# Kernel optimization log

Measured on AMD Instinct MI355X. Metric: run time of the kernel, lower is better.

Reference implementation:

```python
import jax, jax.numpy as jnp
import numpy as np

N = 50000      # nodes
E = 800000     # edges
IN = 128       # in_channels
HID = 64       # hidden_channels (out per head)
H = 4          # heads
ED = 64        # edge_dim
HC = H * HID   # concat output width


def segment_softmax(logits, seg, num_segments):
    # logits: [E, H], softmax over edges sharing the same destination node
    m = jax.ops.segment_max(logits, seg, num_segments=num_segments)
    m = jnp.where(jnp.isfinite(m), m, 0.0)
    e = jnp.exp(logits - m[seg])
    s = jax.ops.segment_sum(e, seg, num_segments=num_segments)
    return e / (s[seg] + 1e-16)


def gatv2_layer(x, src, dst, edge_attr, Wl, bl, Wr, br, We, att, bias):
    # GATv2Conv (PyG, concat=True, negative_slope=0.2), dropout off (eval)
    Hh, C = att.shape
    xl = (x @ Wl + bl).reshape(-1, Hh, C)   # [N,H,C] source transform
    xr = (x @ Wr + br).reshape(-1, Hh, C)   # [N,H,C] target transform
    ee = (edge_attr @ We).reshape(-1, Hh, C)  # [E,H,C]
    m = jax.nn.leaky_relu(xl[src] + xr[dst] + ee, 0.2)  # [E,H,C]
    logits = jnp.einsum('ehc,hc->eh', m, att)           # [E,H]
    alpha = segment_softmax(logits, dst, x.shape[0])    # [E,H]
    out = jax.ops.segment_sum(alpha[:, :, None] * xl[src], dst,
                              num_segments=x.shape[0])  # [N,H,C]
    return out.reshape(x.shape[0], Hh * C) + bias


def setup_inputs() -> dict:
    key = jax.random.key(0)
    ks = jax.random.split(key, 20)
    g = lambda k, shape, s=0.05: (jax.random.normal(k, shape, jnp.float32) * s)
    inp = {
        'x': jax.random.normal(ks[0], (N, IN), jnp.float32),
        'edge_index': jax.random.randint(ks[1], (2, E), 0, N, dtype=jnp.int32),
        'edge_attr': jax.random.normal(ks[2], (E, ED), jnp.float32),
        # layer 1: in_channels -> heads*hidden
        'Wl1': g(ks[3], (IN, HC)), 'bl1': jnp.zeros((HC,), jnp.float32),
        'Wr1': g(ks[4], (IN, HC)), 'br1': jnp.zeros((HC,), jnp.float32),
        'We1': g(ks[5], (ED, HC)),
        'att1': g(ks[6], (H, HID)), 'bias1': jnp.zeros((HC,), jnp.float32),
        # layer 2: heads*hidden -> heads*hidden
        'Wl2': g(ks[7], (HC, HC)), 'bl2': jnp.zeros((HC,), jnp.float32),
        'Wr2': g(ks[8], (HC, HC)), 'br2': jnp.zeros((HC,), jnp.float32),
        'We2': g(ks[9], (ED, HC)),
        'att2': g(ks[10], (H, HID)), 'bias2': jnp.zeros((HC,), jnp.float32),
    }
    return inp


def reference(x, edge_index, edge_attr,
              Wl1, bl1, Wr1, br1, We1, att1, bias1,
              Wl2, bl2, Wr2, br2, We2, att2, bias2):
    src, dst = edge_index[0], edge_index[1]
    h1 = gatv2_layer(x, src, dst, edge_attr, Wl1, bl1, Wr1, br1, We1, att1, bias1)
    h2 = gatv2_layer(h1, src, dst, edge_attr, Wl2, bl2, Wr2, br2, We2, att2, bias2)
    return h2
```

## Files before the change

### kernel.cpp

```cpp
#include <hip/hip_runtime.h>
#include <math.h>

#define NN 50000
#define NE 800000

#define LRELU(v) fmaxf((v), 0.2f * (v))

typedef __attribute__((ext_vector_type(4))) float f32x4;
typedef __attribute__((ext_vector_type(8))) short bf16x8;

static __device__ __forceinline__ unsigned short f2bf(float f) {
  union { float f; unsigned int i; } c; c.f = f;
  unsigned int r = c.i + 0x7fff + ((c.i >> 16) & 1);
  return (unsigned short)(r >> 16);
}
static __device__ __forceinline__ float bflo(unsigned int u) {
  union { unsigned int i; float f; } c; c.i = u << 16; return c.f;
}
static __device__ __forceinline__ float bfhi(unsigned int u) {
  union { unsigned int i; float f; } c; c.i = u & 0xffff0000u; return c.f;
}

__global__ __launch_bounds__(256)
void conv_all(const float* __restrict__ We1, unsigned short* __restrict__ wef1,
              const float* __restrict__ We2, unsigned short* __restrict__ wef2,
              const float* __restrict__ Wl1, unsigned short* __restrict__ wlf1,
              const float* __restrict__ Wr1, unsigned short* __restrict__ wrf1,
              const float* __restrict__ Wl2, unsigned short* __restrict__ wlf2,
              const float* __restrict__ Wr2, unsigned short* __restrict__ wrf2) {
  const int y = blockIdx.y;
  const int g = blockIdx.x * 256 + threadIdx.x;
  if (y < 2) {
    if (g >= 16384) return;
    const float* We = y ? We2 : We1;
    unsigned short* wef = y ? wef2 : wef1;
    const int j = g & 7;
    const int l = (g >> 3) & 63;
    const int t = g >> 9;
    const int n = t & 15, half = t >> 4;
    const int k = half * 32 + (l >> 4) * 8 + j;
    const int c = ((l & 15) >> 2) * 64 + n * 4 + (l & 3);
    wef[g] = f2bf(We[(size_t)k * 256 + c]);
  } else {
    const int K = (y < 4) ? 128 : 256;
    if (g >= K * 256) return;
    const float* W = (y == 2) ? Wl1 : (y == 3) ? Wr1 : (y == 4) ? Wl2 : Wr2;
    unsigned short* wf = (y == 2) ? wlf1 : (y == 3) ? wrf1
                       : (y == 4) ? wlf2 : wrf2;
    const int j = g & 7;
    const int l = (g >> 3) & 63;
    const int fn = g >> 9;
    const int n = fn & 15, ks = fn >> 4;
    const int k = ks * 32 + (l >> 4) * 8 + j;
    const int c = n * 16 + (l & 15);
    wf[g] = f2bf(W[(size_t)k * 256 + c]);
  }
}

template <int KS>
__global__ __launch_bounds__(256)
void gemm_mfma2(const float* __restrict__ A,
                const unsigned short* __restrict__ wfl,
                const float* __restrict__ bl, unsigned short* __restrict__ outl,
                const unsigned short* __restrict__ wfr,
                const float* __restrict__ br, unsigned short* __restrict__ outr) {
  const int tid = threadIdx.x;
  const int w = tid >> 6, l = tid & 63;
  const int lid = l & 15, lg = l >> 4;
  const int row  = blockIdx.x * 64 + w * 16 + lid;
  const bool rowok = row < NN;
  const int rowv = rowok ? row : NN - 1;
  const int K = KS * 32;

  bf16x8 bfr[KS];
  const float* ap = A + (size_t)rowv * K + lg * 8;
#pragma unroll
  for (int ks = 0; ks < KS; ++ks) {
    const float4 v0 = *(const float4*)(ap + ks * 32);
    const float4 v1 = *(const float4*)(ap + ks * 32 + 4);
    bf16x8 b;
    b[0]=f2bf(v0.x); b[1]=f2bf(v0.y); b[2]=f2bf(v0.z); b[3]=f2bf(v0.w);
    b[4]=f2bf(v1.x); b[5]=f2bf(v1.y); b[6]=f2bf(v1.z); b[7]=f2bf(v1.w);
    bfr[ks] = b;
  }

  f32x4 acc[16];

#pragma unroll
  for (int n = 0; n < 16; ++n) acc[n] = (f32x4){0.f, 0.f, 0.f, 0.f};
#pragma unroll
  for (int ks = 0; ks < KS; ++ks)
#pragma unroll
    for (int n = 0; n < 16; ++n) {
      const bf16x8 a = *(const bf16x8*)(wfl + ((size_t)(ks * 16 + n) * 64 + l) * 8);
      acc[n] = __builtin_amdgcn_mfma_f32_16x16x32_bf16(a, bfr[ks], acc[n], 0, 0, 0);
    }
  if (rowok) {
#pragma unroll
    for (int n = 0; n < 16; ++n) {
      const int c0 = n * 16 + lg * 4;
      const float4 bv = *(const float4*)(bl + c0);
      ushort4 o;
      o.x = f2bf(acc[n][0] + bv.x); o.y = f2bf(acc[n][1] + bv.y);
      o.z = f2bf(acc[n][2] + bv.z); o.w = f2bf(acc[n][3] + bv.w);
      *(ushort4*)(outl + (size_t)row * 256 + c0) = o;
    }
  }

#pragma unroll
  for (int n = 0; n < 16; ++n) acc[n] = (f32x4){0.f, 0.f, 0.f, 0.f};
#pragma unroll
  for (int ks = 0; ks < KS; ++ks)
#pragma unroll
    for (int n = 0; n < 16; ++n) {
      const bf16x8 a = *(const bf16x8*)(wfr + ((size_t)(ks * 16 + n) * 64 + l) * 8);
      acc[n] = __builtin_amdgcn_mfma_f32_16x16x32_bf16(a, bfr[ks], acc[n], 0, 0, 0);
    }
  if (rowok) {
#pragma unroll
    for (int n = 0; n < 16; ++n) {
      const int c0 = n * 16 + lg * 4;
      const float4 bv = *(const float4*)(br + c0);
      ushort4 o;
      o.x = f2bf(acc[n][0] + bv.x); o.y = f2bf(acc[n][1] + bv.y);
      o.z = f2bf(acc[n][2] + bv.z); o.w = f2bf(acc[n][3] + bv.w);
      *(ushort4*)(outr + (size_t)row * 256 + c0) = o;
    }
  }
}

__global__ __launch_bounds__(256)
void dst_hist(const int* __restrict__ dst, int* __restrict__ cnt) {
  const int e = blockIdx.x * 256 + threadIdx.x;
  if (e < NE) atomicAdd(&cnt[dst[e]], 1);
}

__global__ __launch_bounds__(1024)
void scan_bsum(const int* __restrict__ cnt, int* __restrict__ bsum, int n) {
  __shared__ int wsum[16];
  const int tid = threadIdx.x;
  const int lane = tid & 63, wid = tid >> 6;
  const int i = blockIdx.x * 1024 + tid;
  int v = (i < n) ? cnt[i] : 0;
#pragma unroll
  for (int off = 32; off >= 1; off >>= 1) v += __shfl_xor(v, off);
  if (lane == 0) wsum[wid] = v;
  __syncthreads();
  if (tid == 0) {
    int s = 0;
#pragma unroll
    for (int k = 0; k < 16; ++k) s += wsum[k];
    bsum[blockIdx.x] = s;
  }
}

__global__ __launch_bounds__(64)
void scan_bsum_scan(int* __restrict__ bsum, int* __restrict__ row_start,
                    int nb, int n) {
  const int lane = threadIdx.x;
  const int v = (lane < nb) ? bsum[lane] : 0;
  int incl = v;
#pragma unroll
  for (int off = 1; off < 64; off <<= 1) {
    const int t = __shfl_up(incl, off);
    if (lane >= off) incl += t;
  }
  if (lane < nb) bsum[lane] = incl - v;
  if (lane == 63) row_start[n] = incl;
}

__global__ __launch_bounds__(1024)
void scan_apply(int* __restrict__ cnt, const int* __restrict__ bsum,
                int* __restrict__ row_start, int n) {
  __shared__ int wsum[16];
  __shared__ int woff[16];
  const int tid = threadIdx.x;
  const int lane = tid & 63, wid = tid >> 6;
  const int i = blockIdx.x * 1024 + tid;
  const int v = (i < n) ? cnt[i] : 0;
  int incl = v;
#pragma unroll
  for (int off = 1; off < 64; off <<= 1) {
    const int t = __shfl_up(incl, off);
    if (lane >= off) incl += t;
  }
  if (lane == 63) wsum[wid] = incl;
  __syncthreads();
  if (wid == 0) {
    const int s = (lane < 16) ? wsum[lane] : 0;
    int si = s;
#pragma unroll
    for (int off = 1; off < 16; off <<= 1) {
      const int t = __shfl_up(si, off);
      if (lane >= off) si += t;
    }
    if (lane < 16) woff[lane] = si - s;
  }
  __syncthreads();
  if (i < n) {
    const int excl = bsum[blockIdx.x] + woff[wid] + incl - v;
    row_start[i] = excl;
    cnt[i] = excl;
  }
}

__global__ __launch_bounds__(256)
void bucket_fill(const int* __restrict__ src, const int* __restrict__ dst,
                 int* __restrict__ cur, int* __restrict__ eid,
                 int* __restrict__ ssrc, int* __restrict__ sdst) {
  const int e = blockIdx.x * 256 + threadIdx.x;
  if (e < NE) {
    const int d = dst[e];
    const int p = atomicAdd(&cur[d], 1);
    eid[p] = e;
    ssrc[p] = src[e];
    sdst[p] = d;
  }
}

__global__ __launch_bounds__(256)
void conv_eab(const float* __restrict__ ea, const int* __restrict__ eid,
              unsigned short* __restrict__ eab) {
  const int g = blockIdx.x * 256 + threadIdx.x;
  const int p = g >> 4, c4 = (g & 15) * 4;
  const int e = eid[p];
  const float4 v = *(const float4*)(ea + (size_t)e * 64 + c4);
  ushort4 o;
  o.x = f2bf(v.x); o.y = f2bf(v.y); o.z = f2bf(v.z); o.w = f2bf(v.w);
  *(ushort4*)(eab + (size_t)p * 64 + c4) = o;
}

template <int EAB>
__global__ __launch_bounds__(128)
void edge_logits_swap(const float* __restrict__ ea,
                      const unsigned short* __restrict__ eab,
                      const unsigned short* __restrict__ wef,
                      const unsigned short* __restrict__ xlb,
                      const unsigned short* __restrict__ xrb,
                      const float* __restrict__ att,
                      const int* __restrict__ eid,
                      const int* __restrict__ ssrc, const int* __restrict__ sdst,
                      float* __restrict__ elog) {
  __shared__ unsigned short sxl[2][16 * 264];

  const int tid = threadIdx.x;
  const int w = tid >> 6, l = tid & 63;
  const int lid = l & 15, lg = l >> 4;
  const int p0 = (blockIdx.x * 2 + w) * 16;
  const int p  = p0 + lid;

  bf16x8 f0, f1;
  if (EAB) {
    f0 = *(const bf16x8*)(eab + (size_t)p * 64 + lg * 8);
    f1 = *(const bf16x8*)(eab + (size_t)p * 64 + 32 + lg * 8);
  } else {
    const int e = eid[p];
    const float* ap = ea + (size_t)e * 64 + lg * 8;
    const float4 v00 = *(const float4*)(ap);
    const float4 v01 = *(const float4*)(ap + 4);
    const float4 v10 = *(const float4*)(ap + 32);
    const float4 v11 = *(const float4*)(ap + 36);
    f0[0]=f2bf(v00.x); f0[1]=f2bf(v00.y); f0[2]=f2bf(v00.z); f0[3]=f2bf(v00.w);
    f0[4]=f2bf(v01.x); f0[5]=f2bf(v01.y); f0[6]=f2bf(v01.z); f0[7]=f2bf(v01.w);
    f1[0]=f2bf(v10.x); f1[1]=f2bf(v10.y); f1[2]=f2bf(v10.z); f1[3]=f2bf(v10.w);
    f1[4]=f2bf(v11.x); f1[5]=f2bf(v11.y); f1[6]=f2bf(v11.z); f1[7]=f2bf(v11.w);
  }

  const int d = sdst[p];
  unsigned short* myxl = sxl[w];

#pragma unroll
  for (int i = 0; i < 8; ++i) {
    const int row  = i * 2 + (l >> 5);
    const int unit = l & 31;
    const int srow = ssrc[p0 + row];
    const uint4 v = *(const uint4*)(xlb + (size_t)srow * 256 + unit * 8);
    *(uint4*)&myxl[row * 264 + unit * 8] = v;
  }

  const unsigned short* xlp  = myxl + lid * 264 + lg * 64;
  const unsigned short* xrp  = xrb + (size_t)d * 256 + lg * 64;
  const float* attp = att + lg * 64;

  float ph = 0.f;
#pragma unroll
  for (int nn = 0; nn < 8; ++nn) {
    const bf16x8 w00 = *(const bf16x8*)(wef + ((size_t)(0  + 2 * nn)     * 64 + l) * 8);
    const bf16x8 w01 = *(const bf16x8*)(wef + ((size_t)(16 + 2 * nn)     * 64 + l) * 8);
    const bf16x8 w10 = *(const bf16x8*)(wef + ((size_t)(0  + 2 * nn + 1) * 64 + l) * 8);
    const bf16x8 w11 = *(const bf16x8*)(wef + ((size_t)(16 + 2 * nn + 1) * 64 + l) * 8);

    f32x4 a0 = (f32x4){0.f,0.f,0.f,0.f}, a1 = (f32x4){0.f,0.f,0.f,0.f};
    a0 = __builtin_amdgcn_mfma_f32_16x16x32_bf16(w00, f0, a0, 0, 0, 0);
    a0 = __builtin_amdgcn_mfma_f32_16x16x32_bf16(w01, f1, a0, 0, 0, 0);
    a1 = __builtin_amdgcn_mfma_f32_16x16x32_bf16(w10, f0, a1, 0, 0, 0);
    a1 = __builtin_amdgcn_mfma_f32_16x16x32_bf16(w11, f1, a1, 0, 0, 0);

    const int c0 = nn * 8;
    const uint4 xu = *(const uint4*)(xlp + c0);
    const uint4 ru = *(const uint4*)(xrp + c0);
    const float4 at0 = *(const float4*)(attp + c0);
    const float4 at1 = *(const float4*)(attp + c0 + 4);
    float v;
    v = a0[0] + bflo(xu.x) + bflo(ru.x); v = LRELU(v); ph += v * at0.x;
    v = a0[1] + bfhi(xu.x) + bfhi(ru.x); v = LRELU(v); ph += v * at0.y;
    v = a0[2] + bflo(xu.y) + bflo(ru.y); v = LRELU(v); ph += v * at0.z;
    v = a0[3] + bfhi(xu.y) + bfhi(ru.y); v = LRELU(v); ph += v * at0.w;
    v = a1[0] + bflo(xu.z) + bflo(ru.z); v = LRELU(v); ph += v * at1.x;
    v = a1[1] + bfhi(xu.z) + bfhi(ru.z); v = LRELU(v); ph += v * at1.y;
    v = a1[2] + bflo(xu.w) + bflo(ru.w); v = LRELU(v); ph += v * at1.z;
    v = a1[3] + bfhi(xu.w) + bfhi(ru.w); v = LRELU(v); ph += v * at1.w;
  }

  elog[(size_t)p * 4 + lg] = expf(ph);
}

__global__ __launch_bounds__(256)
void aggregate(const unsigned short* __restrict__ xlb,
               const float* __restrict__ elog,
               const int* __restrict__ ssrc, const int* __restrict__ row_start,
               const float* __restrict__ bias, float* __restrict__ out) {
  const int wid  = threadIdx.x >> 6;
  const int lane = threadIdx.x & 63;
  const int d    = blockIdx.x * 4 + wid;
  const int h = lane >> 4;
  const int c = lane * 4;
  float ax = 0.f, ay = 0.f, az = 0.f, aw = 0.f;
  float dtot = 0.f;
  const int beg = row_start[d], end = row_start[d + 1];
  int p = beg;
  for (; p + 4 <= end; p += 4) {
    const float e0 = elog[(size_t)(p + 0) * 4 + h];
    const float e1 = elog[(size_t)(p + 1) * 4 + h];
    const float e2 = elog[(size_t)(p + 2) * 4 + h];
    const float e3 = elog[(size_t)(p + 3) * 4 + h];
    const int s0 = ssrc[p + 0], s1 = ssrc[p + 1];
    const int s2 = ssrc[p + 2], s3 = ssrc[p + 3];
    const uint2 x0 = *(const uint2*)(xlb + (size_t)s0 * 256 + c);
    const uint2 x1 = *(const uint2*)(xlb + (size_t)s1 * 256 + c);
    const uint2 x2 = *(const uint2*)(xlb + (size_t)s2 * 256 + c);
    const uint2 x3 = *(const uint2*)(xlb + (size_t)s3 * 256 + c);
    ax += e0*bflo(x0.x) + e1*bflo(x1.x) + e2*bflo(x2.x) + e3*bflo(x3.x);
    ay += e0*bfhi(x0.x) + e1*bfhi(x1.x) + e2*bfhi(x2.x) + e3*bfhi(x3.x);
    az += e0*bflo(x0.y) + e1*bflo(x1.y) + e2*bflo(x2.y) + e3*bflo(x3.y);
    aw += e0*bfhi(x0.y) + e1*bfhi(x1.y) + e2*bfhi(x2.y) + e3*bfhi(x3.y);
    dtot += e0 + e1 + e2 + e3;
  }
  for (; p < end; ++p) {
    const float ev = elog[(size_t)p * 4 + h];
    const int s = ssrc[p];
    const uint2 xv = *(const uint2*)(xlb + (size_t)s * 256 + c);
    ax += ev * bflo(xv.x); ay += ev * bfhi(xv.x);
    az += ev * bflo(xv.y); aw += ev * bfhi(xv.y);
    dtot += ev;
  }
  const float inv = 1.f / (dtot + 1e-16f);
  const float4 bv = *(const float4*)(bias + c);
  float4 o;
  o.x = bv.x + ax * inv; o.y = bv.y + ay * inv;
  o.z = bv.z + az * inv; o.w = bv.w + aw * inv;
  *(float4*)(out + (size_t)d * 256 + c) = o;
}

extern "C" void kernel_launch(void* const* d_in, const int* in_sizes, int n_in,
                              void* d_out, int out_size, void* d_ws, size_t ws_size,
                              hipStream_t stream) {
  const float* x    = (const float*)d_in[0];
  const int*   ei   = (const int*)d_in[1];
  const float* ea   = (const float*)d_in[2];
  const float* Wl1  = (const float*)d_in[3];
  const float* bl1  = (const float*)d_in[4];
  const float* Wr1  = (const float*)d_in[5];
  const float* br1  = (const float*)d_in[6];
  const float* We1  = (const float*)d_in[7];
  const float* att1 = (const float*)d_in[8];
  const float* bias1= (const float*)d_in[9];
  const float* Wl2  = (const float*)d_in[10];
  const float* bl2  = (const float*)d_in[11];
  const float* Wr2  = (const float*)d_in[12];
  const float* br2  = (const float*)d_in[13];
  const float* We2  = (const float*)d_in[14];
  const float* att2 = (const float*)d_in[15];
  const float* bias2= (const float*)d_in[16];

  float* out = (float*)d_out;
  float* ws  = (float*)d_ws;

  float* elog = ws;
  unsigned short* xlb  = (unsigned short*)(elog + (size_t)NE * 4);
  unsigned short* xrb  = xlb + (size_t)NN * 256;
  unsigned short* wef1 = xrb + (size_t)NN * 256;
  unsigned short* wef2 = wef1 + 16384;
  unsigned short* wlf1 = wef2 + 16384;
  unsigned short* wrf1 = wlf1 + 32768;
  unsigned short* wlf2 = wrf1 + 32768;
  unsigned short* wrf2 = wlf2 + 65536;
  int* cur       = (int*)(wrf2 + 65536);
  int* row_start = cur + NN;
  int* bsum      = row_start + NN + 1;
  int* eid       = bsum + 64;
  int* ssrc      = eid + NE;
  int* sdst      = ssrc + NE;
  unsigned short* eab = (unsigned short*)(sdst + NE);
  const size_t need_eab =
      ((char*)(eab + (size_t)NE * 64)) - (char*)d_ws;
  const bool use_eab = ws_size >= need_eab;
  float* h1 = out;

  const int* src = ei;
  const int* dst = ei + NE;

  const int ggrid = (NN + 63) / 64;
  const int egrid = NE / 32;
  const int epb   = (NE + 255) / 256;
  const int agrid = NN / 4;
  const int nb    = (NN + 1023) / 1024;

  hipMemsetAsync(cur, 0, NN * sizeof(int), stream);
  conv_all<<<dim3(256, 6), 256, 0, stream>>>(We1, wef1, We2, wef2,
                                             Wl1, wlf1, Wr1, wrf1,
                                             Wl2, wlf2, Wr2, wrf2);
  dst_hist<<<epb, 256, 0, stream>>>(dst, cur);
  scan_bsum<<<nb, 1024, 0, stream>>>(cur, bsum, NN);
  scan_bsum_scan<<<1, 64, 0, stream>>>(bsum, row_start, nb, NN);
  scan_apply<<<nb, 1024, 0, stream>>>(cur, bsum, row_start, NN);
  bucket_fill<<<epb, 256, 0, stream>>>(src, dst, cur, eid, ssrc, sdst);
  if (use_eab)
    conv_eab<<<NE * 16 / 256, 256, 0, stream>>>(ea, eid, eab);

  gemm_mfma2<4><<<ggrid, 256, 0, stream>>>(x, wlf1, bl1, xlb, wrf1, br1, xrb);
  if (use_eab)
    edge_logits_swap<1><<<egrid, 128, 0, stream>>>(ea, eab, wef1, xlb, xrb,
                                                   att1, eid, ssrc, sdst, elog);
  else
    edge_logits_swap<0><<<egrid, 128, 0, stream>>>(ea, eab, wef1, xlb, xrb,
                                                   att1, eid, ssrc, sdst, elog);
  aggregate<<<agrid, 256, 0, stream>>>(xlb, elog, ssrc, row_start, bias1, h1);

  gemm_mfma2<8><<<ggrid, 256, 0, stream>>>(h1, wlf2, bl2, xlb, wrf2, br2, xrb);
  if (use_eab)
    edge_logits_swap<1><<<egrid, 128, 0, stream>>>(ea, eab, wef2, xlb, xrb,
                                                   att2, eid, ssrc, sdst, elog);
  else
    edge_logits_swap<0><<<egrid, 128, 0, stream>>>(ea, eab, wef2, xlb, xrb,
                                                   att2, eid, ssrc, sdst, elog);
  aggregate<<<agrid, 256, 0, stream>>>(xlb, elog, ssrc, row_start, bias2, out);
}
```

Measured before the change: 693.5 us.

## Store intermediate h1 in bf16 and batch two edge tiles per wave

The first-layer aggregate now writes its output as bf16 into a workspace buffer, and the second-layer GEMM reads bf16 directly instead of loading fp32 and converting. The edge-logit kernel processes two 16-edge tiles per wave, issuing all gathers for both tiles before computing, to hide gather latency. This halves the edge grid and raises register use. The extra workspace buffer could push eab past ws_size and trigger the fallback path.

```diff
diff --git a/kernel.cpp b/kernel.cpp
--- a/kernel.cpp
+++ b/kernel.cpp
@@ -57,9 +57,9 @@
   }
 }
 
-template <int KS>
+template <int KS, int BF>
 __global__ __launch_bounds__(256)
-void gemm_mfma2(const float* __restrict__ A,
+void gemm_mfma2(const void* __restrict__ Av,
                 const unsigned short* __restrict__ wfl,
                 const float* __restrict__ bl, unsigned short* __restrict__ outl,
                 const unsigned short* __restrict__ wfr,
@@ -73,15 +73,24 @@
   const int K = KS * 32;
 
   bf16x8 bfr[KS];
-  const float* ap = A + (size_t)rowv * K + lg * 8;
-#pragma unroll
-  for (int ks = 0; ks < KS; ++ks) {
-    const float4 v0 = *(const float4*)(ap + ks * 32);
-    const float4 v1 = *(const float4*)(ap + ks * 32 + 4);
-    bf16x8 b;
-    b[0]=f2bf(v0.x); b[1]=f2bf(v0.y); b[2]=f2bf(v0.z); b[3]=f2bf(v0.w);
-    b[4]=f2bf(v1.x); b[5]=f2bf(v1.y); b[6]=f2bf(v1.z); b[7]=f2bf(v1.w);
-    bfr[ks] = b;
+  if (BF) {
+    const unsigned short* A = (const unsigned short*)Av;
+    const unsigned short* ap = A + (size_t)rowv * K + lg * 8;
+#pragma unroll
+    for (int ks = 0; ks < KS; ++ks)
+      bfr[ks] = *(const bf16x8*)(ap + ks * 32);
+  } else {
+    const float* A = (const float*)Av;
+    const float* ap = A + (size_t)rowv * K + lg * 8;
+#pragma unroll
+    for (int ks = 0; ks < KS; ++ks) {
+      const float4 v0 = *(const float4*)(ap + ks * 32);
+      const float4 v1 = *(const float4*)(ap + ks * 32 + 4);
+      bf16x8 b;
+      b[0]=f2bf(v0.x); b[1]=f2bf(v0.y); b[2]=f2bf(v0.z); b[3]=f2bf(v0.w);
+      b[4]=f2bf(v1.x); b[5]=f2bf(v1.y); b[6]=f2bf(v1.z); b[7]=f2bf(v1.w);
+      bfr[ks] = b;
+    }
   }
 
   f32x4 acc[16];
@@ -230,58 +239,12 @@
   *(ushort4*)(eab + (size_t)p * 64 + c4) = o;
 }
 
-template <int EAB>
-__global__ __launch_bounds__(128)
-void edge_logits_swap(const float* __restrict__ ea,
-                      const unsigned short* __restrict__ eab,
-                      const unsigned short* __restrict__ wef,
-                      const unsigned short* __restrict__ xlb,
-                      const unsigned short* __restrict__ xrb,
-                      const float* __restrict__ att,
-                      const int* __restrict__ eid,
-                      const int* __restrict__ ssrc, const int* __restrict__ sdst,
-                      float* __restrict__ elog) {
-  __shared__ unsigned short sxl[2][16 * 264];
-
-  const int tid = threadIdx.x;
-  const int w = tid >> 6, l = tid & 63;
-  const int lid = l & 15, lg = l >> 4;
-  const int p0 = (blockIdx.x * 2 + w) * 16;
-  const int p  = p0 + lid;
-
-  bf16x8 f0, f1;
-  if (EAB) {
-    f0 = *(const bf16x8*)(eab + (size_t)p * 64 + lg * 8);
-    f1 = *(const bf16x8*)(eab + (size_t)p * 64 + 32 + lg * 8);
-  } else {
-    const int e = eid[p];
-    const float* ap = ea + (size_t)e * 64 + lg * 8;
-    const float4 v00 = *(const float4*)(ap);
-    const float4 v01 = *(const float4*)(ap + 4);
-    const float4 v10 = *(const float4*)(ap + 32);
-    const float4 v11 = *(const float4*)(ap + 36);
-    f0[0]=f2bf(v00.x); f0[1]=f2bf(v00.y); f0[2]=f2bf(v00.z); f0[3]=f2bf(v00.w);
-    f0[4]=f2bf(v01.x); f0[5]=f2bf(v01.y); f0[6]=f2bf(v01.z); f0[7]=f2bf(v01.w);
-    f1[0]=f2bf(v10.x); f1[1]=f2bf(v10.y); f1[2]=f2bf(v10.z); f1[3]=f2bf(v10.w);
-    f1[4]=f2bf(v11.x); f1[5]=f2bf(v11.y); f1[6]=f2bf(v11.z); f1[7]=f2bf(v11.w);
-  }
-
-  const int d = sdst[p];
-  unsigned short* myxl = sxl[w];
-
-#pragma unroll
-  for (int i = 0; i < 8; ++i) {
-    const int row  = i * 2 + (l >> 5);
-    const int unit = l & 31;
-    const int srow = ssrc[p0 + row];
-    const uint4 v = *(const uint4*)(xlb + (size_t)srow * 256 + unit * 8);
-    *(uint4*)&myxl[row * 264 + unit * 8] = v;
-  }
-
-  const unsigned short* xlp  = myxl + lid * 264 + lg * 64;
-  const unsigned short* xrp  = xrb + (size_t)d * 256 + lg * 64;
-  const float* attp = att + lg * 64;
-
+static __device__ __forceinline__ float edge_epilogue(
+    const unsigned short* __restrict__ xlp,
+    const unsigned short* __restrict__ xrp,
+    const float* __restrict__ attp,
+    const unsigned short* __restrict__ wef,
+    bf16x8 f0, bf16x8 f1, int l) {
   float ph = 0.f;
 #pragma unroll
   for (int nn = 0; nn < 8; ++nn) {
@@ -311,15 +274,113 @@
     v = a1[2] + bflo(xu.w) + bflo(ru.w); v = LRELU(v); ph += v * at1.z;
     v = a1[3] + bfhi(xu.w) + bfhi(ru.w); v = LRELU(v); ph += v * at1.w;
   }
-
-  elog[(size_t)p * 4 + lg] = expf(ph);
-}
-
+  return ph;
+}
+
+template <int EAB>
+__global__ __launch_bounds__(128)
+void edge_logits_swap(const float* __restrict__ ea,
+                      const unsigned short* __restrict__ eab,
+                      const unsigned short* __restrict__ wef,
+                      const unsigned short* __restrict__ xlb,
+                      const unsigned short* __restrict__ xrb,
+                      const float* __restrict__ att,
+                      const int* __restrict__ eid,
+                      const int* __restrict__ ssrc, const int* __restrict__ sdst,
+                      float* __restrict__ elog) {
+  __shared__ unsigned short sxl[2][16 * 264];
+
+  const int tid = threadIdx.x;
+  const int w = tid >> 6, l = tid & 63;
+  const int lid = l & 15, lg = l >> 4;
+  const int base = (blockIdx.x * 2 + w) * 32;
+  const int pA = base + lid;
+  const int pB = base + 16 + lid;
+
+  unsigned short* myxl = sxl[w];
+  const int srow_r = l >> 5;
+  const int unit   = l & 31;
+
+  bf16x8 fA0, fA1;
+  if (EAB) {
+    fA0 = *(const bf16x8*)(eab + (size_t)pA * 64 + lg * 8);
+    fA1 = *(const bf16x8*)(eab + (size_t)pA * 64 + 32 + lg * 8);
+  } else {
+    const int e = eid[pA];
+    const float* ap = ea + (size_t)e * 64 + lg * 8;
+    const float4 v00 = *(const float4*)(ap);
+    const float4 v01 = *(const float4*)(ap + 4);
+    const float4 v10 = *(const float4*)(ap + 32);
+    const float4 v11 = *(const float4*)(ap + 36);
+    fA0[0]=f2bf(v00.x); fA0[1]=f2bf(v00.y); fA0[2]=f2bf(v00.z); fA0[3]=f2bf(v00.w);
+    fA0[4]=f2bf(v01.x); fA0[5]=f2bf(v01.y); fA0[6]=f2bf(v01.z); fA0[7]=f2bf(v01.w);
+    fA1[0]=f2bf(v10.x); fA1[1]=f2bf(v10.y); fA1[2]=f2bf(v10.z); fA1[3]=f2bf(v10.w);
+    fA1[4]=f2bf(v11.x); fA1[5]=f2bf(v11.y); fA1[6]=f2bf(v11.z); fA1[7]=f2bf(v11.w);
+  }
+  const int dA = sdst[pA];
+
+  uint4 gA[8];
+#pragma unroll
+  for (int i = 0; i < 8; ++i) {
+    const int row = i * 2 + srow_r;
+    const int srow = ssrc[base + row];
+    gA[i] = *(const uint4*)(xlb + (size_t)srow * 256 + unit * 8);
+  }
+
+  bf16x8 fB0, fB1;
+  if (EAB) {
+    fB0 = *(const bf16x8*)(eab + (size_t)pB * 64 + lg * 8);
+    fB1 = *(const bf16x8*)(eab + (size_t)pB * 64 + 32 + lg * 8);
+  } else {
+    const int e = eid[pB];
+    const float* ap = ea + (size_t)e * 64 + lg * 8;
+    const float4 v00 = *(const float4*)(ap);
+    const float4 v01 = *(const float4*)(ap + 4);
+    const float4 v10 = *(const float4*)(ap + 32);
+    const float4 v11 = *(const float4*)(ap + 36);
+    fB0[0]=f2bf(v00.x); fB0[1]=f2bf(v00.y); fB0[2]=f2bf(v00.z); fB0[3]=f2bf(v00.w);
+    fB0[4]=f2bf(v01.x); fB0[5]=f2bf(v01.y); fB0[6]=f2bf(v01.z); fB0[7]=f2bf(v01.w);
+    fB1[0]=f2bf(v10.x); fB1[1]=f2bf(v10.y); fB1[2]=f2bf(v10.z); fB1[3]=f2bf(v10.w);
+    fB1[4]=f2bf(v11.x); fB1[5]=f2bf(v11.y); fB1[6]=f2bf(v11.z); fB1[7]=f2bf(v11.w);
+  }
+  const int dB = sdst[pB];
+
+  uint4 gB[8];
+#pragma unroll
+  for (int i = 0; i < 8; ++i) {
+    const int row = i * 2 + srow_r;
+    const int srow = ssrc[base + 16 + row];
+    gB[i] = *(const uint4*)(xlb + (size_t)srow * 256 + unit * 8);
+  }
+
+#pragma unroll
+  for (int i = 0; i < 8; ++i) {
+    const int row = i * 2 + srow_r;
+    *(uint4*)&myxl[row * 264 + unit * 8] = gA[i];
+  }
+  const float phA = edge_epilogue(myxl + lid * 264 + lg * 64,
+                                  xrb + (size_t)dA * 256 + lg * 64,
+                                  att + lg * 64, wef, fA0, fA1, l);
+  elog[(size_t)pA * 4 + lg] = expf(phA);
+
+#pragma unroll
+  for (int i = 0; i < 8; ++i) {
+    const int row = i * 2 + srow_r;
+    *(uint4*)&myxl[row * 264 + unit * 8] = gB[i];
+  }
+  const float phB = edge_epilogue(myxl + lid * 264 + lg * 64,
+                                  xrb + (size_t)dB * 256 + lg * 64,
+                                  att + lg * 64, wef, fB0, fB1, l);
+  elog[(size_t)pB * 4 + lg] = expf(phB);
+}
+
+template <int FINAL>
 __global__ __launch_bounds__(256)
 void aggregate(const unsigned short* __restrict__ xlb,
                const float* __restrict__ elog,
                const int* __restrict__ ssrc, const int* __restrict__ row_start,
-               const float* __restrict__ bias, float* __restrict__ out) {
+               const float* __restrict__ bias, float* __restrict__ outf,
+               unsigned short* __restrict__ outb) {
   const int wid  = threadIdx.x >> 6;
   const int lane = threadIdx.x & 63;
   const int d    = blockIdx.x * 4 + wid;
@@ -359,7 +420,13 @@
   float4 o;
   o.x = bv.x + ax * inv; o.y = bv.y + ay * inv;
   o.z = bv.z + az * inv; o.w = bv.w + aw * inv;
-  *(float4*)(out + (size_t)d * 256 + c) = o;
+  if (FINAL) {
+    *(float4*)(outf + (size_t)d * 256 + c) = o;
+  } else {
+    ushort4 ob;
+    ob.x = f2bf(o.x); ob.y = f2bf(o.y); ob.z = f2bf(o.z); ob.w = f2bf(o.w);
+    *(ushort4*)(outb + (size_t)d * 256 + c) = ob;
+  }
 }
 
 extern "C" void kernel_launch(void* const* d_in, const int* in_sizes, int n_in,
@@ -389,7 +456,8 @@
   float* elog = ws;
   unsigned short* xlb  = (unsigned short*)(elog + (size_t)NE * 4);
   unsigned short* xrb  = xlb + (size_t)NN * 256;
-  unsigned short* wef1 = xrb + (size_t)NN * 256;
+  unsigned short* h1b  = xrb + (size_t)NN * 256;
+  unsigned short* wef1 = h1b + (size_t)NN * 256;
   unsigned short* wef2 = wef1 + 16384;
   unsigned short* wlf1 = wef2 + 16384;
   unsigned short* wrf1 = wlf1 + 32768;
@@ -405,13 +473,12 @@
   const size_t need_eab =
       ((char*)(eab + (size_t)NE * 64)) - (char*)d_ws;
   const bool use_eab = ws_size >= need_eab;
-  float* h1 = out;
 
   const int* src = ei;
   const int* dst = ei + NE;
 
   const int ggrid = (NN + 63) / 64;
-  const int egrid = NE / 32;
+  const int egrid = NE / 64;
   const int epb   = (NE + 255) / 256;
   const int agrid = NN / 4;
   const int nb    = (NN + 1023) / 1024;
@@ -428,21 +495,25 @@
   if (use_eab)
     conv_eab<<<NE * 16 / 256, 256, 0, stream>>>(ea, eid, eab);
 
-  gemm_mfma2<4><<<ggrid, 256, 0, stream>>>(x, wlf1, bl1, xlb, wrf1, br1, xrb);
+  gemm_mfma2<4, 0><<<ggrid, 256, 0, stream>>>(x, wlf1, bl1, xlb,
+                                              wrf1, br1, xrb);
   if (use_eab)
     edge_logits_swap<1><<<egrid, 128, 0, stream>>>(ea, eab, wef1, xlb, xrb,
                                                    att1, eid, ssrc, sdst, elog);
   else
     edge_logits_swap<0><<<egrid, 128, 0, stream>>>(ea, eab, wef1, xlb, xrb,
                                                    att1, eid, ssrc, sdst, elog);
-  aggregate<<<agrid, 256, 0, stream>>>(xlb, elog, ssrc, row_start, bias1, h1);
-
-  gemm_mfma2<8><<<ggrid, 256, 0, stream>>>(h1, wlf2, bl2, xlb, wrf2, br2, xrb);
+  aggregate<0><<<agrid, 256, 0, stream>>>(xlb, elog, ssrc, row_start, bias1,
+                                          nullptr, h1b);
+
+  gemm_mfma2<8, 1><<<ggrid, 256, 0, stream>>>(h1b, wlf2, bl2, xlb,
+                                              wrf2, br2, xrb);
   if (use_eab)
     edge_logits_swap<1><<<egrid, 128, 0, stream>>>(ea, eab, wef2, xlb, xrb,
                                                    att2, eid, ssrc, sdst, elog);
   else
     edge_logits_swap<0><<<egrid, 128, 0, stream>>>(ea, eab, wef2, xlb, xrb,
                                                    att2, eid, ssrc, sdst, elog);
-  aggregate<<<agrid, 256, 0, stream>>>(xlb, elog, ssrc, row_start, bias2, out);
-}
+  aggregate<1><<<agrid, 256, 0, stream>>>(xlb, elog, ssrc, row_start, bias2,
+                                          out, nullptr);
+}
```

New measurement: 679.9 us. About the same (-2.0%).
